# Optimization experiments

Measured on AMD Instinct MI355X. Metric: run time of the kernel, lower is better.

Reference implementation:

```python
import jax, jax.numpy as jnp
import numpy as np

# --- model dims (from init_kwargs: d_model=2048, num_heads=16, d_conv=4, expand_v=2) ---
D_MODEL = 2048
N_HEADS = 16
D_HEAD = D_MODEL // N_HEADS          # 128
EXPAND_V = 2
KEY_DIM = N_HEADS * D_HEAD           # 2048
VALUE_DIM = KEY_DIM * EXPAND_V       # 4096
HEAD_V = D_HEAD * EXPAND_V           # 256
D_CONV = 4
CONV_CH = 2 * KEY_DIM + VALUE_DIM    # 8192 (q,k,v channels)
TOTAL_PROJ = 2 * KEY_DIM + 2 * VALUE_DIM + 2 * N_HEADS  # 12320
SPLITS = np.cumsum([KEY_DIM, KEY_DIM, VALUE_DIM, VALUE_DIM, N_HEADS]).tolist()


def setup_inputs() -> dict:
    key = jax.random.key(0)
    k0, k1, k2, k3 = jax.random.split(key, 4)
    B, L = 2, 2048
    return {
        "hidden_states": jax.random.normal(k0, (B, L, D_MODEL), jnp.float32),
        "W_qkvgba": jax.random.normal(k1, (D_MODEL, TOTAL_PROJ), jnp.float32) * 0.02,
        "W_conv": jax.random.normal(k2, (CONV_CH, D_CONV), jnp.float32) * 0.1,
        "A_log": jax.random.normal(k3, (N_HEADS,), jnp.float32) * 0.1,
        "dt_bias": jnp.zeros((N_HEADS,), jnp.float32),
    }


def _l2norm(x, eps=1e-6):
    return x * jax.lax.rsqrt(jnp.sum(x * x, axis=-1, keepdims=True) + eps)


def reference(hidden_states, W_qkvgba, W_conv, A_log, dt_bias):
    B, L, _ = hidden_states.shape
    # fused qkv / gate / beta / A projection
    proj = hidden_states @ W_qkvgba                      # [B, L, 12320]
    q, k, v, gate, b, A = jnp.split(proj, SPLITS, axis=-1)

    # depthwise causal short conv over q,k,v channels, then SiLU
    qkv = jnp.concatenate([q, k, v], axis=-1)            # [B, L, CONV_CH]
    x = qkv.transpose(0, 2, 1)                           # [B, C, L]
    kern = W_conv[:, None, :]                            # [C, 1, D_CONV]
    y = jax.lax.conv_general_dilated(
        x, kern, window_strides=(1,), padding=[(D_CONV - 1, 0)],
        feature_group_count=CONV_CH)
    y = jax.nn.silu(y).transpose(0, 2, 1)                # [B, L, C]
    q, k, v = jnp.split(y, [KEY_DIM, 2 * KEY_DIM], axis=-1)

    q = q.reshape(B, L, N_HEADS, D_HEAD)
    k = k.reshape(B, L, N_HEADS, D_HEAD)
    v = v.reshape(B, L, N_HEADS, HEAD_V)

    # L2 norm of q,k (use_qk_l2norm_in_kernel=True)
    q = _l2norm(q)
    k = _l2norm(k)
    scale = D_HEAD ** -0.5

    beta = jax.nn.sigmoid(b)                             # [B, L, H]
    g = -jnp.exp(A_log) * jax.nn.softplus(A + dt_bias)   # [B, L, H] (log decay <= 0)

    # gated delta-rule recurrence over time (scan); state S: [B, H, dk, dv]
    qT = q.transpose(1, 0, 2, 3)
    kT = k.transpose(1, 0, 2, 3)
    vT = v.transpose(1, 0, 2, 3)
    gT = g.transpose(1, 0, 2)
    bT = beta.transpose(1, 0, 2)

    def step(S, inp):
        qt, kt, vt, gt, bt = inp
        S = S * jnp.exp(gt)[..., None, None]
        kv = jnp.einsum('bhk,bhkv->bhv', kt, S)          # current memory readout at k
        delta = (vt - kv) * bt[..., None]                # delta-rule error, gated by beta
        S = S + jnp.einsum('bhk,bhv->bhkv', kt, delta)
        ot = jnp.einsum('bhk,bhkv->bhv', qt * scale, S)
        return S, ot

    S0 = jnp.zeros((B, N_HEADS, D_HEAD, HEAD_V), jnp.float32)
    _, oT = jax.lax.scan(step, S0, (qT, kT, vT, gT, bT))
    o = oT.transpose(1, 0, 2, 3)                         # [B, L, H, HEAD_V]

    # output gating: o * silu(gate)
    gate = gate.reshape(B, L, N_HEADS, HEAD_V)
    return o * jax.nn.silu(gate)
```

## Files before the change

### kernel.cpp

```cpp
#include <hip/hip_runtime.h>
#include <hip/hip_bf16.h>
#include <hip/hip_fp16.h>
#include <math.h>

#define L_SEQ 2048
#define DM    2048
#define NH    16
#define DH    128
#define HVD   256
#define NPROJ 12320
#define QKVW  8192
#define GW    4128

#define NTILE_N 97
#define KSTEPS  64

typedef _Float16 v8h __attribute__((ext_vector_type(8)));
typedef float f32x4 __attribute__((ext_vector_type(4)));

__device__ __forceinline__ void gload_lds16(const void* g, void* l) {
  __builtin_amdgcn_global_load_lds((const __attribute__((address_space(1))) void*)g,
                                   (__attribute__((address_space(3))) void*)l, 16, 0, 0);
}

__device__ __forceinline__ void splitw(float x, unsigned short& h, unsigned short& l) {
  _Float16 hh = (_Float16)x;
  _Float16 ll = (_Float16)(x - (float)hh);
  h = *(unsigned short*)&hh;
  l = *(unsigned short*)&ll;
}
__device__ __forceinline__ float h2f(unsigned short u) {
  return (float)(*(_Float16*)&u);
}

#define MFMA3(acc, ah, al, bh_, bl_)                                          \
  acc = __builtin_amdgcn_mfma_f32_16x16x32_f16(ah, bh_, acc, 0, 0, 0);        \
  acc = __builtin_amdgcn_mfma_f32_16x16x32_f16(ah, bl_, acc, 0, 0, 0);        \
  acc = __builtin_amdgcn_mfma_f32_16x16x32_f16(al, bh_, acc, 0, 0, 0);

__global__ __launch_bounds__(256) void pack_A_k(const float* __restrict__ H, _Float16* __restrict__ Ap) {
  const int mtile = blockIdx.x >> 6, kstep = blockIdx.x & 63;
  const size_t base = (size_t)blockIdx.x * 2 * 4096;
#pragma unroll
  for (int it = 0; it < 2; ++it) {
    int s = threadIdx.x + it * 256;
    int g = s >> 7, r = s & 127;
    const float* src = H + ((size_t)(mtile * 128 + r)) * 2048 + kstep * 32 + g * 8;
    float4 x0 = *(const float4*)src;
    float4 x1 = *(const float4*)(src + 4);
    float xs[8] = {x0.x, x0.y, x0.z, x0.w, x1.x, x1.y, x1.z, x1.w};
    v8h hi, lo;
#pragma unroll
    for (int j = 0; j < 8; ++j) {
      float v = xs[j] * 16.f;
      _Float16 h = (_Float16)v;
      hi[j] = h;
      lo[j] = (_Float16)(v - (float)h);
    }
    *(v8h*)(Ap + base + g * 1024 + r * 8) = hi;
    *(v8h*)(Ap + base + 4096 + g * 1024 + r * 8) = lo;
  }
}

__global__ __launch_bounds__(256) void pack_B_k(const float* __restrict__ W, _Float16* __restrict__ Bp) {
  const int ntile = blockIdx.x >> 6, kstep = blockIdx.x & 63;
  const size_t base = (size_t)blockIdx.x * 2 * 4096;
#pragma unroll
  for (int it = 0; it < 2; ++it) {
    int s = threadIdx.x + it * 256;
    int g = s >> 7, col = s & 127;
    int n = ntile * 128 + col;
    v8h hi, lo;
#pragma unroll
    for (int j = 0; j < 8; ++j) {
      int k = kstep * 32 + g * 8 + j;
      float v = (n < NPROJ) ? W[(size_t)k * NPROJ + n] * 1024.f : 0.f;
      _Float16 h = (_Float16)v;
      hi[j] = h;
      lo[j] = (_Float16)(v - (float)h);
    }
    *(v8h*)(Bp + base + g * 1024 + col * 8) = hi;
    *(v8h*)(Bp + base + 4096 + g * 1024 + col * 8) = lo;
  }
}

__global__ __launch_bounds__(256) void gemm_mfma_k(const _Float16* __restrict__ Ap,
                                                   const _Float16* __restrict__ Bp,
                                                   float* __restrict__ Cq,
                                                   float* __restrict__ Cg) {
  __shared__ _Float16 lds[2][16384];
  const int tid = threadIdx.x;
  const int mtile = blockIdx.x & 31;
  const int ntile = blockIdx.x >> 5;
  const int wid = tid >> 6, lane = tid & 63;
  const int wm = wid >> 1, wn = wid & 1;
  const int lrow = lane & 15, g = lane >> 4;

  f32x4 acc[4][4];
#pragma unroll
  for (int i = 0; i < 4; ++i)
#pragma unroll
    for (int j = 0; j < 4; ++j) acc[i][j] = (f32x4){0.f, 0.f, 0.f, 0.f};

  const int aoff = (wm * 64 + lrow) * 8 + g * 1024;
  const int boff = (wn * 64 + lrow) * 8 + g * 1024;

  const _Float16* Asrc = Ap + ((size_t)(mtile * KSTEPS) * 2) * 4096 + tid * 8;
  const _Float16* Bsrc = Bp + ((size_t)(ntile * KSTEPS) * 2) * 4096 + tid * 8;

#define STAGE(KS, BUF)                                                         \
  {                                                                            \
    const _Float16* An_ = Asrc + (size_t)(KS) * 8192;                          \
    const _Float16* Bn_ = Bsrc + (size_t)(KS) * 8192;                          \
    _Pragma("unroll")                                                          \
    for (int r = 0; r < 4; ++r) {                                              \
      gload_lds16(An_ + r * 2048, &lds[BUF][r * 2048 + tid * 8]);              \
      gload_lds16(Bn_ + r * 2048, &lds[BUF][8192 + r * 2048 + tid * 8]);       \
    }                                                                          \
  }

  STAGE(0, 0);
  STAGE(1, 1);

  for (int kstep = 0; kstep < KSTEPS; ++kstep) {
    const int p = kstep & 1;
    if (kstep + 1 < KSTEPS) {
      asm volatile("s_waitcnt vmcnt(8)" ::: "memory");
    } else {
      asm volatile("s_waitcnt vmcnt(0)" ::: "memory");
    }
    __builtin_amdgcn_sched_barrier(0);
    __builtin_amdgcn_s_barrier();
    __builtin_amdgcn_sched_barrier(0);

    v8h ah[4], al[4], bh[4], bl[4];
#pragma unroll
    for (int f = 0; f < 4; ++f) {
      ah[f] = *(const v8h*)&lds[p][aoff + f * 128];
      al[f] = *(const v8h*)&lds[p][4096 + aoff + f * 128];
      bh[f] = *(const v8h*)&lds[p][8192 + boff + f * 128];
      bl[f] = *(const v8h*)&lds[p][12288 + boff + f * 128];
    }
#pragma unroll
    for (int fm = 0; fm < 4; ++fm)
#pragma unroll
      for (int fn = 0; fn < 4; ++fn) {
        acc[fm][fn] = __builtin_amdgcn_mfma_f32_16x16x32_f16(ah[fm], bh[fn], acc[fm][fn], 0, 0, 0);
        acc[fm][fn] = __builtin_amdgcn_mfma_f32_16x16x32_f16(ah[fm], bl[fn], acc[fm][fn], 0, 0, 0);
        acc[fm][fn] = __builtin_amdgcn_mfma_f32_16x16x32_f16(al[fm], bh[fn], acc[fm][fn], 0, 0, 0);
      }
    __builtin_amdgcn_sched_barrier(0);
    __builtin_amdgcn_s_barrier();
    __builtin_amdgcn_sched_barrier(0);
    if (kstep + 2 < KSTEPS) STAGE(kstep + 2, p);
  }
#undef STAGE

  const float sc = 1.f / 16384.f;
#pragma unroll
  for (int fm = 0; fm < 4; ++fm) {
    int row = mtile * 128 + wm * 64 + fm * 16 + g * 4;
#pragma unroll
    for (int fn = 0; fn < 4; ++fn) {
      int col = ntile * 128 + wn * 64 + fn * 16 + lrow;
      if (col < QKVW) {
#pragma unroll
        for (int r = 0; r < 4; ++r)
          Cq[(size_t)(row + r) * QKVW + col] = acc[fm][fn][r] * sc;
      } else if (col < NPROJ) {
        int lcol = col - QKVW;
#pragma unroll
        for (int r = 0; r < 4; ++r)
          Cg[(size_t)(row + r) * GW + lcol] = acc[fm][fn][r] * sc;
      }
    }
  }
}

__global__ __launch_bounds__(64) void conv_qk_k(
    const float* __restrict__ projQKV, const float* __restrict__ Wc,
    _Float16* __restrict__ qh, _Float16* __restrict__ ql,
    _Float16* __restrict__ kh, _Float16* __restrict__ kl)
{
  const int b = blockIdx.z, hg = blockIdx.y, tc = blockIdx.x;
  const int lane = threadIdx.x;
  const int ch = hg * 128 + lane * 2;
  float4 Wa = *(const float4*)(Wc + (size_t)ch * 4);
  float4 Wb = *(const float4*)(Wc + (size_t)ch * 4 + 4);
  const int t0 = tc * 64;
  const float* P = projQKV + (size_t)b * L_SEQ * QKVW + ch;
  float2 w0 = make_float2(0.f, 0.f), w1 = w0, w2 = w0;
  if (t0 >= 3) w0 = *(const float2*)(P + (size_t)(t0 - 3) * QKVW);
  if (t0 >= 2) w1 = *(const float2*)(P + (size_t)(t0 - 2) * QKVW);
  if (t0 >= 1) w2 = *(const float2*)(P + (size_t)(t0 - 1) * QKVW);
  const bool isq = hg < 16;
  const int h = isq ? hg : hg - 16;
  _Float16* dh = (isq ? qh : kh) + (((size_t)b * NH + h) * L_SEQ) * 128;
  _Float16* dl = (isq ? ql : kl) + (((size_t)b * NH + h) * L_SEQ) * 128;
  const float sc = (isq ? 0.08838834764831845f : 1.f) * 1024.f;
  for (int t = t0; t < t0 + 64; ++t) {
    float2 x = *(const float2*)(P + (size_t)t * QKVW);
    float y0 = w0.x * Wa.x + w1.x * Wa.y + w2.x * Wa.z + x.x * Wa.w;
    float y1 = w0.y * Wb.x + w1.y * Wb.y + w2.y * Wb.z + x.y * Wb.w;
    w0 = w1; w1 = w2; w2 = x;
    y0 = y0 / (1.f + expf(-y0));
    y1 = y1 / (1.f + expf(-y1));
    float ss = y0 * y0 + y1 * y1;
#pragma unroll
    for (int off = 1; off < 64; off <<= 1) ss += __shfl_xor(ss, off);
    float nrm = sc / sqrtf(ss + 1e-6f);
    unsigned short h0, l0, h1, l1;
    splitw(y0 * nrm, h0, l0);
    splitw(y1 * nrm, h1, l1);
    int idx = t * 128 + ((lane * 2) ^ ((t & 7) << 3));
    *(unsigned int*)&dh[idx] = (unsigned int)h0 | ((unsigned int)h1 << 16);
    *(unsigned int*)&dl[idx] = (unsigned int)l0 | ((unsigned int)l1 << 16);
  }
}

__global__ __launch_bounds__(256) void conv_v_k(
    const float* __restrict__ projQKV, const float* __restrict__ Wc,
    float* __restrict__ vn)
{
  const int b = blockIdx.z, cg = blockIdx.y, tc = blockIdx.x;
  const int vc = (cg * 256 + threadIdx.x) * 4;
  const int ch = 4096 + vc;
  float4 Wv0 = *(const float4*)(Wc + (size_t)ch * 4);
  float4 Wv1 = *(const float4*)(Wc + (size_t)ch * 4 + 4);
  float4 Wv2 = *(const float4*)(Wc + (size_t)ch * 4 + 8);
  float4 Wv3 = *(const float4*)(Wc + (size_t)ch * 4 + 12);
  const int t0 = tc * 64;
  const float* P = projQKV + (size_t)b * L_SEQ * QKVW + ch;
  float4 w0 = make_float4(0.f, 0.f, 0.f, 0.f), w1 = w0, w2 = w0;
  if (t0 >= 3) w0 = *(const float4*)(P + (size_t)(t0 - 3) * QKVW);
  if (t0 >= 2) w1 = *(const float4*)(P + (size_t)(t0 - 2) * QKVW);
  if (t0 >= 1) w2 = *(const float4*)(P + (size_t)(t0 - 1) * QKVW);
  const int h = vc >> 8, vcol = vc & 255;
  float* dst = vn + (((size_t)b * NH + h) * L_SEQ) * HVD + vcol;
  for (int t = t0; t < t0 + 64; ++t) {
    float4 x = *(const float4*)(P + (size_t)t * QKVW);
    float4 y;
    y.x = w0.x * Wv0.x + w1.x * Wv0.y + w2.x * Wv0.z + x.x * Wv0.w;
    y.y = w0.y * Wv1.x + w1.y * Wv1.y + w2.y * Wv1.z + x.y * Wv1.w;
    y.z = w0.z * Wv2.x + w1.z * Wv2.y + w2.z * Wv2.z + x.z * Wv2.w;
    y.w = w0.w * Wv3.x + w1.w * Wv3.y + w2.w * Wv3.z + x.w * Wv3.w;
    w0 = w1; w1 = w2; w2 = x;
    y.x = y.x / (1.f + expf(-y.x));
    y.y = y.y / (1.f + expf(-y.y));
    y.z = y.z / (1.f + expf(-y.z));
    y.w = y.w / (1.f + expf(-y.w));
    *(float4*)(dst + (size_t)t * HVD) = y;
  }
}

__global__ __launch_bounds__(256) void beta_g_k(
    const float* __restrict__ projGate, const float* __restrict__ A_log,
    const float* __restrict__ dt_bias, float* __restrict__ beta, float* __restrict__ g_out)
{
  int idx = blockIdx.x * 256 + threadIdx.x;
  if (idx >= 2 * NH * L_SEQ) return;
  int t = idx & (L_SEQ - 1);
  int h = (idx >> 11) & (NH - 1);
  int b = idx >> 15;
  size_t row = (size_t)(b * L_SEQ + t) * GW;
  float bv = projGate[row + 4096 + h];
  float av = projGate[row + 4112 + h];
  float be = 1.f / (1.f + expf(-bv));
  float xx = av + dt_bias[h];
  float sp = (xx > 20.f) ? xx : log1pf(expf(xx));
  float g = -expf(A_log[h]) * sp;
  beta[idx] = be;
  g_out[idx] = g;
}

__global__ __launch_bounds__(256) void p1_k(
    const _Float16* __restrict__ kh_g, const _Float16* __restrict__ kl_g,
    const _Float16* __restrict__ qh_g, const _Float16* __restrict__ ql_g,
    const float* __restrict__ g_arr, const float* __restrict__ beta_arr,
    _Float16* __restrict__ Tg_h, _Float16* __restrict__ Tg_l,
    _Float16* __restrict__ Hg_h, _Float16* __restrict__ Hg_l,
    _Float16* __restrict__ KTg_h, _Float16* __restrict__ KTg_l,
    float* __restrict__ coefG)
{
  __shared__ _Float16 Kh[8192], Kl[8192];
  __shared__ _Float16 QS[16384];
  __shared__ float lc[64], be[64], kw[64];
  _Float16* Qh = QS;
  _Float16* Ql = QS + 8192;
  float* Am = (float*)QS;
  float* Tm = Am + 4096;
  const int cid = blockIdx.x, bh = cid >> 5, ch = cid & 31, t0 = ch * 64;
  const int tid = threadIdx.x, w = tid >> 6, lane = tid & 63, lr = lane & 15, g16 = lane >> 4;

  const size_t gb = ((size_t)bh * 2048 + t0) * 128;
#pragma unroll
  for (int l = 0; l < 4; ++l) {
    int i = (tid + l * 256) * 8;
    gload_lds16(kh_g + gb + i, &Kh[i]);
    gload_lds16(kl_g + gb + i, &Kl[i]);
    gload_lds16(qh_g + gb + i, &Qh[i]);
    gload_lds16(ql_g + gb + i, &Ql[i]);
  }
  if (tid < 64) {
    float x = g_arr[(size_t)bh * 2048 + t0 + tid];
#pragma unroll
    for (int off = 1; off < 64; off <<= 1) { float y = __shfl_up(x, off); if (tid >= off) x += y; }
    lc[tid] = x;
    float x63 = __shfl(x, 63);
    float b_ = beta_arr[(size_t)bh * 2048 + t0 + tid];
    be[tid] = b_;
    kw[tid] = expf(x63 - x);
    float ca = expf(x);
    coefG[(size_t)cid * 192 + tid] = ca;
    coefG[(size_t)cid * 192 + 64 + tid] = b_;
    coefG[(size_t)cid * 192 + 128 + tid] = b_ * ca;
  }
  __syncthreads();
  const float ds20 = 1.f / 1048576.f;
  const int arow = w * 16 + lr, swa = (arow & 7) << 3;
  f32x4 gacc[4];
  for (int nt = 0; nt < 4; ++nt) {
    f32x4 acc = (f32x4){0.f, 0.f, 0.f, 0.f};
    int nrow = nt * 16 + lr, swn = (nrow & 7) << 3;
#pragma unroll
    for (int ks = 0; ks < 4; ++ks) {
      int c = ks * 32 + g16 * 8;
      v8h ah = *(const v8h*)&Kh[arow * 128 + (c ^ swa)];
      v8h al = *(const v8h*)&Kl[arow * 128 + (c ^ swa)];
      v8h bhh = *(const v8h*)&Kh[nrow * 128 + (c ^ swn)];
      v8h bll = *(const v8h*)&Kl[nrow * 128 + (c ^ swn)];
      MFMA3(acc, ah, al, bhh, bll);
    }
    gacc[nt] = acc;
  }
  for (int nt = 0; nt < 4; ++nt) {
    f32x4 acc = (f32x4){0.f, 0.f, 0.f, 0.f};
    int nrow = nt * 16 + lr, swn = (nrow & 7) << 3;
#pragma unroll
    for (int ks = 0; ks < 4; ++ks) {
      int c = ks * 32 + g16 * 8;
      v8h ah = *(const v8h*)&Qh[arow * 128 + (c ^ swa)];
      v8h al = *(const v8h*)&Ql[arow * 128 + (c ^ swa)];
      v8h bhh = *(const v8h*)&Kh[nrow * 128 + (c ^ swn)];
      v8h bll = *(const v8h*)&Kl[nrow * 128 + (c ^ swn)];
      MFMA3(acc, ah, al, bhh, bll);
    }
    int s_ = nt * 16 + lr;
#pragma unroll
    for (int r = 0; r < 4; ++r) {
      int t = w * 16 + g16 * 4 + r;
      float hv = (s_ <= t) ? acc[r] * ds20 * expf(lc[t] - lc[s_]) : 0.f;
      unsigned short hh, ll; splitw(hv * 16384.f, hh, ll);
      size_t go = (size_t)cid * 4096 + t * 64 + (s_ ^ ((t & 7) << 3));
      *(unsigned short*)&Hg_h[go] = hh;
      *(unsigned short*)&Hg_l[go] = ll;
    }
  }
  __syncthreads();
  for (int nt = 0; nt < 4; ++nt) {
    int s_ = nt * 16 + lr;
#pragma unroll
    for (int r = 0; r < 4; ++r) {
      int t = w * 16 + g16 * 4 + r;
      float av = (s_ < t) ? gacc[nt][r] * ds20 * be[t] * expf(lc[t] - lc[s_]) : 0.f;
      Am[t * 64 + s_] = av;
    }
  }
#pragma unroll
  for (int l = 0; l < 16; ++l) { int s2 = tid + l * 256; Tm[s2] = ((s2 >> 6) == (s2 & 63)) ? 1.f : 0.f; }
  for (int s = tid; s < 8192; s += 256) {
    int feat = s >> 6, t = s & 63;
    int ki = t * 128 + (feat ^ ((t & 7) << 3));
    float kvv = ((float)Kh[ki] + (float)Kl[ki]) * kw[t];
    unsigned short hh, ll; splitw(kvv, hh, ll);
    size_t go = (size_t)cid * 8192 + feat * 64 + (t ^ ((feat & 7) << 3));
    *(unsigned short*)&KTg_h[go] = hh;
    *(unsigned short*)&KTg_l[go] = ll;
  }
  __syncthreads();
  if (w == 0) {
    int j = lane;
    for (int t = 1; t < 64; ++t) {
      float sum = 0.f;
      for (int s = 0; s < t; ++s) sum = fmaf(Am[t * 64 + s], Tm[s * 64 + j], sum);
      Tm[t * 64 + j] = ((j == t) ? 1.f : 0.f) - sum;
    }
  }
  __syncthreads();
#pragma unroll
  for (int l = 0; l < 16; ++l) {
    int s2 = tid + l * 256;
    int t = s2 >> 6, sc_ = s2 & 63;
    unsigned short hh, ll; splitw(Tm[s2] * 256.f, hh, ll);
    size_t go = (size_t)cid * 4096 + t * 64 + (sc_ ^ ((t & 7) << 3));
    *(unsigned short*)&Tg_h[go] = hh;
    *(unsigned short*)&Tg_l[go] = ll;
  }
}

__global__ __launch_bounds__(256) void p2_k(
    const _Float16* __restrict__ qh_g, const _Float16* __restrict__ ql_g,
    const _Float16* __restrict__ kh_g, const _Float16* __restrict__ kl_g,
    const float* __restrict__ vn, const float* __restrict__ projGate,
    const _Float16* __restrict__ Tg_h, const _Float16* __restrict__ Tg_l,
    const _Float16* __restrict__ Hg_h, const _Float16* __restrict__ Hg_l,
    const _Float16* __restrict__ KTg_h, const _Float16* __restrict__ KTg_l,
    const float* __restrict__ coefG, float* __restrict__ out)
{
  __shared__ _Float16 St_h[4096], St_l[4096];
  __shared__ _Float16 KQ0[8192], KQ1[8192];
  __shared__ _Float16 KK0[8192], KK1[8192];
  __shared__ _Float16 KTs_h[8192], KTs_l[8192];
  __shared__ _Float16 Ts_h[4096], Ts_l[4096];
  __shared__ _Float16 Hs_h[4096], Hs_l[4096];
  __shared__ float cf[192];

  const int blk = blockIdx.x;
  const int vb = blk >> 5, bh = blk & 31;
  const int b = bh >> 4, h = bh & 15, v0 = vb * 32;
  const int tid = threadIdx.x, w = tid >> 6, lane = tid & 63, lr = lane & 15, g16 = lane >> 4;

  _Float16* BT_h = &KQ0[0];
  _Float16* BT_l = &KQ0[4096];
  _Float16* UT_h = &KQ1[0];
  _Float16* UT_l = &KQ1[4096];

#pragma unroll
  for (int l = 0; l < 8; ++l) { ((unsigned int*)St_h)[tid + l * 256] = 0u; }
#pragma unroll
  for (int l = 0; l < 8; ++l) { ((unsigned int*)St_l)[tid + l * 256] = 0u; }

  const float* gp = projGate + ((size_t)b * 2048) * GW + h * 256 + v0;
  const float i2_16 = 1.f / 65536.f;
  const float i2_20 = 1.f / 1048576.f;
  const float uscale = 1.f / 256.f;
  const float sscale = 64.f / 65536.f;

  for (int ch = 0; ch < 32; ++ch) {
    const int cid = bh * 32 + ch, t0 = ch * 64;
    {
      const _Float16* th = Tg_h + (size_t)cid * 4096;
      const _Float16* tl = Tg_l + (size_t)cid * 4096;
      const _Float16* hh = Hg_h + (size_t)cid * 4096;
      const _Float16* hl = Hg_l + (size_t)cid * 4096;
      const _Float16* kth = KTg_h + (size_t)cid * 8192;
      const _Float16* ktl = KTg_l + (size_t)cid * 8192;
      const size_t gb = ((size_t)bh * 2048 + t0) * 128;
#pragma unroll
      for (int l = 0; l < 2; ++l) {
        int i = (tid + l * 256) * 8;
        gload_lds16(th + i, &Ts_h[i]);
        gload_lds16(tl + i, &Ts_l[i]);
        gload_lds16(hh + i, &Hs_h[i]);
        gload_lds16(hl + i, &Hs_l[i]);
      }
#pragma unroll
      for (int l = 0; l < 4; ++l) {
        int i = (tid + l * 256) * 8;
        gload_lds16(kth + i, &KTs_h[i]);
        gload_lds16(ktl + i, &KTs_l[i]);
        gload_lds16(qh_g + gb + i, &KQ0[i]);
        gload_lds16(ql_g + gb + i, &KQ1[i]);
        gload_lds16(kh_g + gb + i, &KK0[i]);
        gload_lds16(kl_g + gb + i, &KK1[i]);
      }
      if (tid < 48) gload_lds16(coefG + (size_t)cid * 192 + tid * 4, &cf[tid * 4]);
    }
    float Vv[2][4];
#pragma unroll
    for (int nt = 0; nt < 2; ++nt)
#pragma unroll
      for (int r = 0; r < 4; ++r)
        Vv[nt][r] = vn[((size_t)bh * 2048 + t0 + w * 16 + g16 * 4 + r) * 256 + v0 + nt * 16 + lr];
    __syncthreads();
    const float cc = cf[63];
    const int arow = w * 16 + lr, swa = (arow & 7) << 3;
    f32x4 Oacc[2];
    {
      for (int nt = 0; nt < 2; ++nt) {
        f32x4 acc = (f32x4){0.f, 0.f, 0.f, 0.f};
        const int n = nt * 16 + lr, swn = (n & 7) << 3;
#pragma unroll
        for (int ks = 0; ks < 4; ++ks) {
          int c = ks * 32 + g16 * 8;
          v8h ah = *(const v8h*)&KQ0[arow * 128 + (c ^ swa)];
          v8h al = *(const v8h*)&KQ1[arow * 128 + (c ^ swa)];
          v8h bhh = *(const v8h*)&St_h[n * 128 + (c ^ swn)];
          v8h bll = *(const v8h*)&St_l[n * 128 + (c ^ swn)];
          MFMA3(acc, ah, al, bhh, bll);
        }
        Oacc[nt] = acc;
      }
      float4 cav = *(float4*)&cf[w * 16 + g16 * 4];
#pragma unroll
      for (int nt = 0; nt < 2; ++nt) {
        Oacc[nt][0] *= cav.x * 16.f; Oacc[nt][1] *= cav.y * 16.f;
        Oacc[nt][2] *= cav.z * 16.f; Oacc[nt][3] *= cav.w * 16.f;
      }
    }
    ushort4 pBh[2], pBl[2];
    {
      float4 cb1v = *(float4*)&cf[64 + w * 16 + g16 * 4];
      float4 cb2v = *(float4*)&cf[128 + w * 16 + g16 * 4];
      for (int nt = 0; nt < 2; ++nt) {
        f32x4 acc = (f32x4){0.f, 0.f, 0.f, 0.f};
        const int n = nt * 16 + lr, swn = (n & 7) << 3;
#pragma unroll
        for (int ks = 0; ks < 4; ++ks) {
          int c = ks * 32 + g16 * 8;
          v8h ah = *(const v8h*)&KK0[arow * 128 + (c ^ swa)];
          v8h al = *(const v8h*)&KK1[arow * 128 + (c ^ swa)];
          v8h bhh = *(const v8h*)&St_h[n * 128 + (c ^ swn)];
          v8h bll = *(const v8h*)&St_l[n * 128 + (c ^ swn)];
          MFMA3(acc, ah, al, bhh, bll);
        }
        float cb1a[4] = {cb1v.x, cb1v.y, cb1v.z, cb1v.w};
        float cb2a[4] = {cb2v.x, cb2v.y, cb2v.z, cb2v.w};
        unsigned short* ph = (unsigned short*)&pBh[nt];
        unsigned short* pl = (unsigned short*)&pBl[nt];
#pragma unroll
        for (int r = 0; r < 4; ++r) {
          float kv = acc[r] * i2_16;
          float Bv = cb1a[r] * Vv[nt][r] - cb2a[r] * kv;
          splitw(Bv * 64.f, ph[r], pl[r]);
        }
      }
    }
    __syncthreads();
    {
      const int tb = w * 16 + g16 * 4;
      for (int nt = 0; nt < 2; ++nt) {
        const int n = nt * 16 + lr, swn = (n & 7) << 3;
        int ad = n * 64 + (tb ^ swn);
        *(ushort4*)&BT_h[ad] = pBh[nt];
        *(ushort4*)&BT_l[ad] = pBl[nt];
      }
    }
    __syncthreads();
    {
      const int tb = w * 16 + g16 * 4;
      for (int nt = 0; nt < 2; ++nt) {
        f32x4 acc = (f32x4){0.f, 0.f, 0.f, 0.f};
        const int n = nt * 16 + lr, swn = (n & 7) << 3;
#pragma unroll
        for (int ks = 0; ks < 2; ++ks) {
          int c = ks * 32 + g16 * 8;
          v8h ah = *(const v8h*)&Ts_h[arow * 64 + (c ^ swa)];
          v8h al = *(const v8h*)&Ts_l[arow * 64 + (c ^ swa)];
          v8h bhh = *(const v8h*)&BT_h[n * 64 + (c ^ swn)];
          v8h bll = *(const v8h*)&BT_l[n * 64 + (c ^ swn)];
          MFMA3(acc, ah, al, bhh, bll);
        }
        ushort4 H, L;
        unsigned short* ph = (unsigned short*)&H;
        unsigned short* pl = (unsigned short*)&L;
#pragma unroll
        for (int r = 0; r < 4; ++r) splitw(acc[r] * uscale, ph[r], pl[r]);
        int ad = n * 64 + (tb ^ swn);
        *(ushort4*)&UT_h[ad] = H;
        *(ushort4*)&UT_l[ad] = L;
      }
    }
    __syncthreads();
    {
      for (int nt = 0; nt < 2; ++nt) {
        const int n = nt * 16 + lr, swn = (n & 7) << 3;
#pragma unroll
        for (int ks = 0; ks < 2; ++ks) {
          int c = ks * 32 + g16 * 8;
          v8h ah = *(const v8h*)&Hs_h[arow * 64 + (c ^ swa)];
          v8h al = *(const v8h*)&Hs_l[arow * 64 + (c ^ swa)];
          v8h bhh = *(const v8h*)&UT_h[n * 64 + (c ^ swn)];
          v8h bll = *(const v8h*)&UT_l[n * 64 + (c ^ swn)];
          MFMA3(Oacc[nt], ah, al, bhh, bll);
        }
      }
      for (int nt = 0; nt < 2; ++nt) {
        const int n = nt * 16 + lr;
#pragma unroll
        for (int r = 0; r < 4; ++r) {
          int t = t0 + w * 16 + g16 * 4 + r;
          float Ov = Oacc[nt][r] * i2_20;
          float gv = gp[(size_t)t * GW + n];
          out[((size_t)b * 2048 + t) * 4096 + h * 256 + v0 + n] = Ov * (gv / (1.f + expf(-gv)));
        }
      }
      const float cc1024 = cc * 1024.f;
#pragma unroll
      for (int m2 = w * 2; m2 < w * 2 + 2; ++m2) {
        const int ar2 = m2 * 16 + lr, swa2 = (ar2 & 7) << 3;
        const int fb = m2 * 16 + g16 * 4;
        for (int nt = 0; nt < 2; ++nt) {
          const int n = nt * 16 + lr, swn = (n & 7) << 3;
          int sad = n * 128 + (fb ^ swn);
          ushort4 sh4 = *(ushort4*)&St_h[sad];
          ushort4 sl4 = *(ushort4*)&St_l[sad];
          f32x4 acc;
          acc[0] = cc1024 * (h2f(sh4.x) + h2f(sl4.x));
          acc[1] = cc1024 * (h2f(sh4.y) + h2f(sl4.y));
          acc[2] = cc1024 * (h2f(sh4.z) + h2f(sl4.z));
          acc[3] = cc1024 * (h2f(sh4.w) + h2f(sl4.w));
#pragma unroll
          for (int ks = 0; ks < 2; ++ks) {
            int c = ks * 32 + g16 * 8;
            v8h ah = *(const v8h*)&KTs_h[ar2 * 64 + (c ^ swa2)];
            v8h al = *(const v8h*)&KTs_l[ar2 * 64 + (c ^ swa2)];
            v8h bhh = *(const v8h*)&UT_h[n * 64 + (c ^ swn)];
            v8h bll = *(const v8h*)&UT_l[n * 64 + (c ^ swn)];
            MFMA3(acc, ah, al, bhh, bll);
          }
          ushort4 H, L;
          unsigned short* ph = (unsigned short*)&H;
          unsigned short* pl = (unsigned short*)&L;
#pragma unroll
          for (int r = 0; r < 4; ++r) splitw(acc[r] * sscale, ph[r], pl[r]);
          *(ushort4*)&St_h[sad] = H;
          *(ushort4*)&St_l[sad] = L;
        }
      }
    }
    __syncthreads();
  }
}

extern "C" void kernel_launch(void* const* d_in, const int* in_sizes, int n_in,
                              void* d_out, int out_size, void* d_ws, size_t ws_size,
                              hipStream_t stream) {
  const float* hidden  = (const float*)d_in[0];
  const float* W       = (const float*)d_in[1];
  const float* Wc      = (const float*)d_in[2];
  const float* A_log   = (const float*)d_in[3];
  const float* dt_bias = (const float*)d_in[4];
  float* out = (float*)d_out;

  char* ws = (char*)d_ws;
  _Float16* Ap = (_Float16*)ws;
  _Float16* Bp = (_Float16*)(ws + (size_t)33554432);
  _Float16* qh = (_Float16*)ws;
  _Float16* ql = (_Float16*)(ws + (size_t)16777216);
  _Float16* kh = (_Float16*)(ws + (size_t)33554432);
  _Float16* kl = (_Float16*)(ws + (size_t)50331648);
  float* vn    = (float*)(ws + (size_t)67108864);
  float* g_arr = (float*)(ws + (size_t)134217728);
  float* beta  = (float*)(ws + (size_t)134479872);
  float* projQKV = (float*)(ws + (size_t)135266304);
  char*  tb0 = ws + (size_t)135266304;
  _Float16* Tg_h  = (_Float16*)tb0;
  _Float16* Tg_l  = (_Float16*)(tb0 + (size_t)8388608);
  _Float16* Hg_h  = (_Float16*)(tb0 + (size_t)16777216);
  _Float16* Hg_l  = (_Float16*)(tb0 + (size_t)25165824);
  _Float16* KTg_h = (_Float16*)(tb0 + (size_t)33554432);
  _Float16* KTg_l = (_Float16*)(tb0 + (size_t)50331648);
  float*    coefG = (float*)   (tb0 + (size_t)67108864);
  float* projGate = (float*)(ws + (size_t)269484032);

  pack_A_k<<<32 * KSTEPS, 256, 0, stream>>>(hidden, Ap);
  pack_B_k<<<NTILE_N * KSTEPS, 256, 0, stream>>>(W, Bp);
  gemm_mfma_k<<<32 * NTILE_N, 256, 0, stream>>>(Ap, Bp, projQKV, projGate);

  conv_qk_k<<<dim3(32, 32, 2), 64, 0, stream>>>(projQKV, Wc, qh, ql, kh, kl);
  conv_v_k<<<dim3(32, 4, 2), 256, 0, stream>>>(projQKV, Wc, vn);
  beta_g_k<<<(2 * NH * L_SEQ + 255) / 256, 256, 0, stream>>>(projGate, A_log, dt_bias, beta, g_arr);

  p1_k<<<1024, 256, 0, stream>>>(kh, kl, qh, ql, g_arr, beta, Tg_h, Tg_l, Hg_h, Hg_l, KTg_h, KTg_l, coefG);
  p2_k<<<256, 256, 0, stream>>>(qh, ql, kh, kl, vn, projGate, Tg_h, Tg_l, Hg_h, Hg_l, KTg_h, KTg_l, coefG, out);
}
```

Measured before the change: 1.022 ms.

## Add 256x256-tile projection GEMM kernel with remainder tile on old kernel

Adds a 512-thread GEMM kernel that computes 256x256 output tiles from pairs of the existing packed 128-wide A and B panels, so each loaded panel is reused across twice as many outputs. It covers the first 96 N-tiles, and the old 128x128 kernel now takes an ntile offset to handle only the last partial tile. The aim is to cut global and LDS traffic per MFMA in the split-fp16 projection GEMM. The cost is 64 KB per buffer of LDS double buffering, a 128-register accumulator array per thread, fewer blocks, and an extra kernel launch.

```diff
diff --git a/kernel.cpp b/kernel.cpp
--- a/kernel.cpp
+++ b/kernel.cpp
@@ -84,14 +84,104 @@
   }
 }
 
+__global__ __launch_bounds__(512, 2) void gemm256_k(const _Float16* __restrict__ Ap,
+                                                    const _Float16* __restrict__ Bp,
+                                                    float* __restrict__ Cq,
+                                                    float* __restrict__ Cg) {
+  __shared__ _Float16 lds[2][32768];
+  const int tid = threadIdx.x;
+  const int supM = blockIdx.x & 15;
+  const int supN = blockIdx.x >> 4;
+  const int w = tid >> 6, lane = tid & 63;
+  const int wm = w >> 2, wn = w & 3;
+  const int lr = lane & 15, g16 = lane >> 4;
+
+  f32x4 acc[8][4];
+#pragma unroll
+  for (int i = 0; i < 8; ++i)
+#pragma unroll
+    for (int j = 0; j < 4; ++j) acc[i][j] = (f32x4){0.f, 0.f, 0.f, 0.f};
+
+  const size_t Ab0 = (size_t)(2 * supM) * KSTEPS * 8192;
+  const size_t Ab1 = Ab0 + (size_t)KSTEPS * 8192;
+  const size_t Bb0 = (size_t)(2 * supN) * KSTEPS * 8192;
+  const size_t Bb1 = Bb0 + (size_t)KSTEPS * 8192;
+  const int so = tid * 8;
+
+#define STG(KS, BUF)                                                           \
+  {                                                                            \
+    const size_t ko = (size_t)(KS) * 8192;                                     \
+    gload_lds16(Ap + Ab0 + ko + so,        &lds[BUF][so]);                     \
+    gload_lds16(Ap + Ab0 + ko + so + 4096, &lds[BUF][so + 4096]);              \
+    gload_lds16(Ap + Ab1 + ko + so,        &lds[BUF][8192 + so]);              \
+    gload_lds16(Ap + Ab1 + ko + so + 4096, &lds[BUF][8192 + so + 4096]);       \
+    gload_lds16(Bp + Bb0 + ko + so,        &lds[BUF][16384 + so]);             \
+    gload_lds16(Bp + Bb0 + ko + so + 4096, &lds[BUF][16384 + so + 4096]);      \
+    gload_lds16(Bp + Bb1 + ko + so,        &lds[BUF][24576 + so]);             \
+    gload_lds16(Bp + Bb1 + ko + so + 4096, &lds[BUF][24576 + so + 4096]);      \
+  }
+
+  STG(0, 0);
+  asm volatile("s_waitcnt vmcnt(0)" ::: "memory");
+  __builtin_amdgcn_sched_barrier(0);
+  __builtin_amdgcn_s_barrier();
+  __builtin_amdgcn_sched_barrier(0);
+
+  const int aoffB = wm * 8192 + lr * 8 + g16 * 1024;
+  const int boffB = 16384 + (wn >> 1) * 8192 + ((wn & 1) * 64 + lr) * 8 + g16 * 1024;
+
+  for (int kstep = 0; kstep < KSTEPS; ++kstep) {
+    const int p = kstep & 1;
+    if (kstep + 1 < KSTEPS) STG(kstep + 1, p ^ 1);
+
+    v8h ah[8], al[8];
+#pragma unroll
+    for (int mb = 0; mb < 8; ++mb) {
+      ah[mb] = *(const v8h*)&lds[p][aoffB + mb * 128];
+      al[mb] = *(const v8h*)&lds[p][aoffB + mb * 128 + 4096];
+    }
+#pragma unroll
+    for (int nt = 0; nt < 4; ++nt) {
+      v8h bh = *(const v8h*)&lds[p][boffB + nt * 128];
+      v8h bl = *(const v8h*)&lds[p][boffB + nt * 128 + 4096];
+#pragma unroll
+      for (int mb = 0; mb < 8; ++mb) {
+        MFMA3(acc[mb][nt], ah[mb], al[mb], bh, bl);
+      }
+    }
+    asm volatile("s_waitcnt vmcnt(0)" ::: "memory");
+    __builtin_amdgcn_sched_barrier(0);
+    __builtin_amdgcn_s_barrier();
+    __builtin_amdgcn_sched_barrier(0);
+  }
+#undef STG
+
+  const float sc = 1.f / 16384.f;
+#pragma unroll
+  for (int mb = 0; mb < 8; ++mb) {
+#pragma unroll
+    for (int nt = 0; nt < 4; ++nt) {
+      int col = supN * 256 + wn * 64 + nt * 16 + lr;
+#pragma unroll
+      for (int r = 0; r < 4; ++r) {
+        int row = supM * 256 + wm * 128 + mb * 16 + g16 * 4 + r;
+        float v = acc[mb][nt][r] * sc;
+        if (col < QKVW) Cq[(size_t)row * QKVW + col] = v;
+        else            Cg[(size_t)row * GW + (col - QKVW)] = v;
+      }
+    }
+  }
+}
+
 __global__ __launch_bounds__(256) void gemm_mfma_k(const _Float16* __restrict__ Ap,
                                                    const _Float16* __restrict__ Bp,
                                                    float* __restrict__ Cq,
-                                                   float* __restrict__ Cg) {
+                                                   float* __restrict__ Cg,
+                                                   int ntile_base) {
   __shared__ _Float16 lds[2][16384];
   const int tid = threadIdx.x;
   const int mtile = blockIdx.x & 31;
-  const int ntile = blockIdx.x >> 5;
+  const int ntile = ntile_base + (blockIdx.x >> 5);
   const int wid = tid >> 6, lane = tid & 63;
   const int wm = wid >> 1, wn = wid & 1;
   const int lrow = lane & 15, g = lane >> 4;
@@ -656,7 +746,8 @@
 
   pack_A_k<<<32 * KSTEPS, 256, 0, stream>>>(hidden, Ap);
   pack_B_k<<<NTILE_N * KSTEPS, 256, 0, stream>>>(W, Bp);
-  gemm_mfma_k<<<32 * NTILE_N, 256, 0, stream>>>(Ap, Bp, projQKV, projGate);
+  gemm256_k<<<16 * 48, 512, 0, stream>>>(Ap, Bp, projQKV, projGate);
+  gemm_mfma_k<<<32, 256, 0, stream>>>(Ap, Bp, projQKV, projGate, 96);
 
   conv_qk_k<<<dim3(32, 32, 2), 64, 0, stream>>>(projQKV, Wc, qh, ql, kh, kl);
   conv_v_k<<<dim3(32, 4, 2), 256, 0, stream>>>(projQKV, Wc, vn);
```

New measurement: 971.4 us. 5.0% less time.
